# Kernel optimization log

Hardware: AMD Instinct MI355X
Metric: run time of the kernel (lower is better)

Reference implementation:

```python
import jax, jax.numpy as jnp
import numpy as np

FEATURE_DIM = 512
DEPTH = 128
NUM_CLASSES = 1000


def setup_inputs() -> dict:
    key = jax.random.key(0)
    ks = jax.random.split(key, 9)
    s = 1.0 / np.sqrt(FEATURE_DIM)
    sd = 1.0 / np.sqrt(DEPTH)
    return {
        "x": jax.random.normal(ks[0], (8, 2048, FEATURE_DIM), dtype=jnp.float32),
        "Wq": jax.random.uniform(ks[1], (FEATURE_DIM, DEPTH), jnp.float32, -s, s),
        "bq": jax.random.uniform(ks[2], (DEPTH,), jnp.float32, -s, s),
        "Wk": jax.random.uniform(ks[3], (FEATURE_DIM, DEPTH), jnp.float32, -s, s),
        "bk": jax.random.uniform(ks[4], (DEPTH,), jnp.float32, -s, s),
        "Wv": jax.random.uniform(ks[5], (FEATURE_DIM, DEPTH), jnp.float32, -s, s),
        "bv": jax.random.uniform(ks[6], (DEPTH,), jnp.float32, -s, s),
        "Wl": jax.random.uniform(ks[7], (DEPTH, NUM_CLASSES), jnp.float32, -sd, sd),
        "bl": jax.random.uniform(ks[8], (NUM_CLASSES,), jnp.float32, -sd, sd),
    }


def reference(x, Wq, bq, Wk, bk, Wv, bv, Wl, bl):
    # q,k,v: [B,S,depth]
    q = jnp.einsum("bsf,fd->bsd", x, Wq) + bq
    k = jnp.einsum("bsf,fd->bsd", x, Wk) + bk
    v = jnp.einsum("bsf,fd->bsd", x, Wv) + bv
    # NOTE: original applies no 1/sqrt(depth) scaling
    logit = jnp.einsum("bqd,bkd->bqk", q, k)  # [B,S,S]
    attn = jax.nn.softmax(logit, axis=2)
    attn_out = jnp.einsum("bqk,bkd->bqd", attn, v)  # [B,S,depth]
    out = jnp.einsum("bsd,dc->bsc", attn_out, Wl) + bl  # [B,S,C]
    return out.mean(axis=1)  # [B,C]
```

## Files before the change

### kernel.cpp

```cpp
#include <hip/hip_runtime.h>
#include <stdint.h>

#define NB 8
#define SS 2048
#define FF 512
#define DD 128
#define CC 1000
#define KC 8
#define CHUNK (SS / KC)

typedef __attribute__((ext_vector_type(8))) short bf16x8;
typedef __attribute__((ext_vector_type(4))) float f32x4;
typedef __attribute__((ext_vector_type(4))) unsigned int u32x4;

__device__ __forceinline__ short f2bf(float f) {
    uint32_t u;
    __builtin_memcpy(&u, &f, 4);
    u = (u + 0x7fffu + ((u >> 16) & 1u)) >> 16;
    return (short)u;
}
__device__ __forceinline__ float bf2f(short h) {
    uint32_t u = ((uint32_t)(uint16_t)h) << 16;
    float f;
    __builtin_memcpy(&f, &u, 4);
    return f;
}
__device__ __forceinline__ uint32_t cvtpk(float a, float b) {
    uint32_t r;
    asm("v_cvt_pk_bf16_f32 %0, %1, %2" : "=v"(r) : "v"(a), "v"(b));
    return r;
}
__device__ __forceinline__ void async16(const void* g, void* l) {
    __builtin_amdgcn_global_load_lds(
        (const __attribute__((address_space(1))) uint32_t*)g,
        (__attribute__((address_space(3))) uint32_t*)l, 16, 0, 0);
}

__global__ void prep(const float* __restrict__ Wq, const float* __restrict__ Wk,
                     const float* __restrict__ Wv, short* __restrict__ Wt)
{
    int id = blockIdx.x * 256 + threadIdx.x;
    int w = id >> 16, rem = id & 65535;
    int n = rem >> 9, kx = rem & 511;
    const float* Wsrc = (w == 0) ? Wq : (w == 1) ? Wk : Wv;
    Wt[w * 65536 + n * 512 + kx] = f2bf(Wsrc[kx * 128 + n]);
}

__global__ __launch_bounds__(256) void qkv_proj(
    const float* __restrict__ x, const short* __restrict__ Wt,
    const float* __restrict__ bq, const float* __restrict__ bk, const float* __restrict__ bv,
    short* __restrict__ qo, short* __restrict__ ko, short* __restrict__ vo)
{
    __shared__ __align__(16) short As[2][128 * 64];
    __shared__ __align__(16) short Bs[2][128 * 64];

    const int m0   = blockIdx.x * 128;
    const int mat  = blockIdx.y;
    const int tid  = threadIdx.x;
    const int wave = tid >> 6, lane = tid & 63;
    const int quad = lane >> 4, l16 = lane & 15;
    const int wr = wave >> 1, wc = wave & 1;

    const short* Wm = Wt + mat * 65536;

    f32x4 acc[4][4];
    for (int i = 0; i < 4; i++)
        for (int j = 0; j < 4; j++) acc[i][j] = (f32x4){0.f, 0.f, 0.f, 0.f};

    const int sr = lane >> 3;
    const int sc = (lane & 7) ^ (sr & 7);

    float4 a0[4], a1[4];

#define A_LOAD(kk)                                                          \
    for (int i = 0; i < 4; i++) {                                           \
        int ins = wave * 4 + i;                                             \
        int r = ins * 8 + sr;                                               \
        const float4* s4 = (const float4*)(x + (size_t)(m0 + r) * 512 + (kk) + sc * 8); \
        a0[i] = s4[0]; a1[i] = s4[1];                                       \
    }
#define A_WRITE(buf)                                                        \
    for (int i = 0; i < 4; i++) {                                           \
        int ins = wave * 4 + i;                                             \
        u32x4 p;                                                            \
        p[0] = cvtpk(a0[i].x, a0[i].y);                                     \
        p[1] = cvtpk(a0[i].z, a0[i].w);                                     \
        p[2] = cvtpk(a1[i].x, a1[i].y);                                     \
        p[3] = cvtpk(a1[i].z, a1[i].w);                                     \
        *(u32x4*)&As[buf][ins * 512 + lane * 8] = p;                        \
    }
#define B_STAGE(buf, kk)                                                    \
    for (int i = 0; i < 4; i++) {                                           \
        int ins = wave * 4 + i;                                             \
        int r = ins * 8 + sr;                                               \
        async16(Wm + r * 512 + (kk) + sc * 8, &Bs[buf][ins * 512]);         \
    }

    A_LOAD(0)
    B_STAGE(0, 0)
    A_WRITE(0)
    __syncthreads();

    int cur = 0;
    for (int t = 0; t < 8; t++) {
        if (t < 7) {
            A_LOAD((t + 1) * 64)
            B_STAGE(cur ^ 1, (t + 1) * 64)
        }

        for (int kc = 0; kc < 2; kc++) {
            bf16x8 af[4], bfr[4];
            for (int mt = 0; mt < 4; mt++) {
                int R = wr * 64 + mt * 16 + l16, cc = kc * 4 + quad;
                af[mt] = *(const bf16x8*)&As[cur][(R * 8 + (cc ^ (R & 7))) * 8];
            }
            for (int nt = 0; nt < 4; nt++) {
                int R = wc * 64 + nt * 16 + l16, cc = kc * 4 + quad;
                bfr[nt] = *(const bf16x8*)&Bs[cur][(R * 8 + (cc ^ (R & 7))) * 8];
            }
            for (int mt = 0; mt < 4; mt++)
                for (int nt = 0; nt < 4; nt++)
                    acc[mt][nt] = __builtin_amdgcn_mfma_f32_16x16x32_bf16(
                        af[mt], bfr[nt], acc[mt][nt], 0, 0, 0);
        }
        if (t < 7) { A_WRITE(cur ^ 1) }
        __syncthreads();
        cur ^= 1;
    }
#undef A_LOAD
#undef A_WRITE
#undef B_STAGE

    const float* bias = (mat == 0) ? bq : (mat == 1) ? bk : bv;
    short* outp = (mat == 0) ? qo : (mat == 1) ? ko : vo;
    for (int mt = 0; mt < 4; mt++) {
        int grow_base = m0 + wr * 64 + mt * 16 + quad * 4;
        for (int nt = 0; nt < 4; nt++) {
            int col = wc * 64 + nt * 16 + l16;
            float bb = bias[col];
            for (int r = 0; r < 4; r++)
                outp[(grow_base + r) * 128 + col] = f2bf(acc[mt][nt][r] + bb);
        }
    }
}

__global__ __launch_bounds__(256) void attn_l(
    const short* __restrict__ q, const short* __restrict__ k,
    float* __restrict__ l_part, float* __restrict__ accum)
{
    __shared__ __align__(16) short ks[2][64 * 128];

    const int b  = blockIdx.y;
    const int q0 = blockIdx.x * 128;
    const int lq = blockIdx.z;
    const int c0 = lq * CHUNK;
    const int tid  = threadIdx.x;
    const int wave = tid >> 6, lane = tid & 63;
    const int quad = lane >> 4, l16 = lane & 15;

    if (blockIdx.x == 0 && blockIdx.y == 0 && blockIdx.z == 0) {
        accum[tid] = 0.f; accum[256 + tid] = 0.f;
        accum[512 + tid] = 0.f; accum[768 + tid] = 0.f;
    }

    bf16x8 qf[2][4];
    for (int m = 0; m < 2; m++)
        for (int c = 0; c < 4; c++)
            qf[m][c] = *(const bf16x8*)(q + (b * 2048 + q0 + wave * 32 + m * 16 + l16) * 128
                                          + c * 32 + quad * 8);

    float lsum[2][4] = {{0.f,0.f,0.f,0.f},{0.f,0.f,0.f,0.f}};
    const int krl = lane >> 4;

#define K_STAGE(buf, s0)                                                     \
    for (int i = 0; i < 4; i++) {                                            \
        int ik = wave * 4 + i;                                               \
        int kr = ik * 4 + krl;                                               \
        int kc8 = (lane & 15) ^ (kr & 15);                                   \
        async16(k + (b * 2048 + (s0) + kr) * 128 + kc8 * 8, &ks[buf][ik * 512]); \
    }

    K_STAGE(0, c0)
    __syncthreads();

    int cur = 0;
    for (int t = 0; t < CHUNK / 64; t++) {
        if (t < CHUNK / 64 - 1) { K_STAGE(cur ^ 1, c0 + (t + 1) * 64) }

        for (int ct = 0; ct < 4; ct++) {
            f32x4 Sf[2];
            Sf[0] = (f32x4){0.f,0.f,0.f,0.f};
            Sf[1] = (f32x4){0.f,0.f,0.f,0.f};
            int R = ct * 16 + l16;
            __builtin_amdgcn_s_setprio(1);
            for (int c = 0; c < 4; c++) {
                int cc = c * 4 + quad;
                bf16x8 kb = *(const bf16x8*)&ks[cur][(R * 16 + (cc ^ l16)) * 8];
                for (int m = 0; m < 2; m++)
                    Sf[m] = __builtin_amdgcn_mfma_f32_16x16x32_bf16(
                        qf[m][c], kb, Sf[m], 0, 0, 0);
            }
            __builtin_amdgcn_s_setprio(0);
            for (int m = 0; m < 2; m++)
                for (int r = 0; r < 4; r++)
                    lsum[m][r] += __expf(Sf[m][r] - 10.0f);
        }
        __syncthreads();
        cur ^= 1;
    }

    for (int m = 0; m < 2; m++)
        for (int r = 0; r < 4; r++) {
            float lv = lsum[m][r];
            lv += __shfl_xor(lv, 1);
            lv += __shfl_xor(lv, 2);
            lv += __shfl_xor(lv, 4);
            lv += __shfl_xor(lv, 8);
            if (l16 == 0)
                l_part[(lq * 8 + b) * 2048 + q0 + wave * 32 + m * 16 + quad * 4 + r] = lv;
        }
}

__global__ __launch_bounds__(256) void attn_w(
    const short* __restrict__ q, const short* __restrict__ k,
    const float* __restrict__ l_part, float* __restrict__ w_part)
{
    __shared__ __align__(16) short ks[2][64 * 128];
    __shared__ float wl[4][256];

    const int b  = blockIdx.y;
    const int qt = blockIdx.x;
    const int q0 = qt * 128;
    const int lq = blockIdx.z;
    const int c0 = lq * CHUNK;
    const int tid  = threadIdx.x;
    const int wave = tid >> 6, lane = tid & 63;
    const int quad = lane >> 4, l16 = lane & 15;

    bf16x8 qf[2][4];
    for (int m = 0; m < 2; m++)
        for (int c = 0; c < 4; c++)
            qf[m][c] = *(const bf16x8*)(q + (b * 2048 + q0 + wave * 32 + m * 16 + l16) * 128
                                          + c * 32 + quad * 8);

    float linv[2][4];
    for (int m = 0; m < 2; m++)
        for (int r = 0; r < 4; r++) {
            int row = q0 + wave * 32 + m * 16 + quad * 4 + r;
            float lt = 0.f;
            for (int kc = 0; kc < KC; kc++) lt += l_part[(kc * 8 + b) * 2048 + row];
            linv[m][r] = 1.0f / lt;
        }

    const int krl = lane >> 4;

    K_STAGE(0, c0)
    __syncthreads();

    int cur = 0;
    for (int t = 0; t < CHUNK / 64; t++) {
        if (t < CHUNK / 64 - 1) { K_STAGE(cur ^ 1, c0 + (t + 1) * 64) }
        int s0 = c0 + t * 64;

        for (int ct = 0; ct < 4; ct++) {
            f32x4 Sf[2];
            Sf[0] = (f32x4){0.f,0.f,0.f,0.f};
            Sf[1] = (f32x4){0.f,0.f,0.f,0.f};
            int R = ct * 16 + l16;
            __builtin_amdgcn_s_setprio(1);
            for (int c = 0; c < 4; c++) {
                int cc = c * 4 + quad;
                bf16x8 kb = *(const bf16x8*)&ks[cur][(R * 16 + (cc ^ l16)) * 8];
                for (int m = 0; m < 2; m++)
                    Sf[m] = __builtin_amdgcn_mfma_f32_16x16x32_bf16(
                        qf[m][c], kb, Sf[m], 0, 0, 0);
            }
            __builtin_amdgcn_s_setprio(0);
            float cs = 0.f;
            for (int m = 0; m < 2; m++)
                for (int r = 0; r < 4; r++)
                    cs += __expf(Sf[m][r] - 10.0f) * linv[m][r];
            cs += __shfl_xor(cs, 16);
            cs += __shfl_xor(cs, 32);
            if (quad == 0) wl[wave][(s0 - c0) + ct * 16 + l16] = cs;
        }
        __syncthreads();
        cur ^= 1;
    }
#undef K_STAGE

    {
        float s = wl[0][tid] + wl[1][tid] + wl[2][tid] + wl[3][tid];
        w_part[(qt * 8 + b) * 2048 + c0 + tid] = s;
    }
}

__global__ __launch_bounds__(256) void wv(
    const float* __restrict__ w_part, const short* __restrict__ vo,
    float* __restrict__ accum)
{
    __shared__ float wsh[128];
    __shared__ float red[16][129];
    const int b    = blockIdx.x;
    const int slab = blockIdx.y;
    const int tid  = threadIdx.x;

    if (tid < 128) {
        int s = slab * 128 + tid;
        float wsum = 0.f;
        for (int qt = 0; qt < 16; qt++) wsum += w_part[(qt * 8 + b) * 2048 + s];
        wsh[tid] = wsum;
    }
    __syncthreads();

    const int dgrp = tid & 15, sgrp = tid >> 4;
    const int d0 = dgrp * 8;
    float a[8] = {0.f,0.f,0.f,0.f,0.f,0.f,0.f,0.f};
    for (int i = 0; i < 8; i++) {
        int sl = sgrp * 8 + i;
        bf16x8 v = *(const bf16x8*)(vo + (size_t)(b * 2048 + slab * 128 + sl) * 128 + d0);
        float w = wsh[sl];
        for (int j = 0; j < 8; j++) a[j] += w * bf2f(v[j]);
    }
    for (int j = 0; j < 8; j++) red[sgrp][d0 + j] = a[j];
    __syncthreads();

    if (tid < 128) {
        float s = 0.f;
        for (int g = 0; g < 16; g++) s += red[g][tid];
        atomicAdd(&accum[b * 128 + tid], s);
    }
}

__global__ void final_proj(const float* __restrict__ accum, const float* __restrict__ Wl,
                           const float* __restrict__ bl, float* __restrict__ out)
{
    int id = blockIdx.x * 256 + threadIdx.x;
    if (id >= NB * CC) return;
    int b = id / CC, c = id % CC;
    float s = 0.f;
    for (int d = 0; d < 128; d++)
        s += accum[b * 128 + d] * Wl[d * 1000 + c];
    out[id] = s * (1.0f / 2048.0f) + bl[c];
}

extern "C" void kernel_launch(void* const* d_in, const int* in_sizes, int n_in,
                              void* d_out, int out_size, void* d_ws, size_t ws_size,
                              hipStream_t stream) {
    const float* x  = (const float*)d_in[0];
    const float* Wq = (const float*)d_in[1];
    const float* bq = (const float*)d_in[2];
    const float* Wk = (const float*)d_in[3];
    const float* bk = (const float*)d_in[4];
    const float* Wv = (const float*)d_in[5];
    const float* bv = (const float*)d_in[6];
    const float* Wl = (const float*)d_in[7];
    const float* bl = (const float*)d_in[8];
    float* out = (float*)d_out;

    char* ws = (char*)d_ws;
    short* qo     = (short*)(ws);
    short* ko     = (short*)(ws + 4194304);
    short* vo     = (short*)(ws + 8388608);
    short* Wt     = (short*)(ws + 12582912);
    float* l_part = (float*)(ws + 12976128);
    float* w_part = (float*)(ws + 13500416);
    float* acc    = (float*)(ws + 14548992);

    prep<<<768, 256, 0, stream>>>(Wq, Wk, Wv, Wt);
    qkv_proj<<<dim3(128, 3), 256, 0, stream>>>(x, Wt, bq, bk, bv, qo, ko, vo);
    attn_l<<<dim3(16, 8, KC), 256, 0, stream>>>(qo, ko, l_part, acc);
    attn_w<<<dim3(16, 8, KC), 256, 0, stream>>>(qo, ko, l_part, w_part);
    wv<<<dim3(8, 16), 256, 0, stream>>>(w_part, vo, acc);
    final_proj<<<(NB * CC + 255) / 256, 256, 0, stream>>>(acc, Wl, bl, out);
}
```

Measured before the change: 146.1 us.

## Fuse Q/K/V projections into one kernel sharing each x tile across all three

```diff
diff --git a/kernel.cpp b/kernel.cpp
--- a/kernel.cpp
+++ b/kernel.cpp
@@ -46,54 +46,44 @@
     Wt[w * 65536 + n * 512 + kx] = f2bf(Wsrc[kx * 128 + n]);
 }
 
-__global__ __launch_bounds__(256) void qkv_proj(
+__global__ __launch_bounds__(512) void qkv_mega(
     const float* __restrict__ x, const short* __restrict__ Wt,
     const float* __restrict__ bq, const float* __restrict__ bk, const float* __restrict__ bv,
     short* __restrict__ qo, short* __restrict__ ko, short* __restrict__ vo)
 {
-    __shared__ __align__(16) short As[2][128 * 64];
-    __shared__ __align__(16) short Bs[2][128 * 64];
-
-    const int m0   = blockIdx.x * 128;
-    const int mat  = blockIdx.y;
+    __shared__ __align__(16) short As[2][64 * 64];
+    __shared__ __align__(16) short Bs[2][384 * 64];
+
+    const int m0   = blockIdx.x * 64;
     const int tid  = threadIdx.x;
     const int wave = tid >> 6, lane = tid & 63;
     const int quad = lane >> 4, l16 = lane & 15;
-    const int wr = wave >> 1, wc = wave & 1;
-
-    const short* Wm = Wt + mat * 65536;
-
-    f32x4 acc[4][4];
+
+    f32x4 acc[4][3];
     for (int i = 0; i < 4; i++)
-        for (int j = 0; j < 4; j++) acc[i][j] = (f32x4){0.f, 0.f, 0.f, 0.f};
-
-    const int sr = lane >> 3;
-    const int sc = (lane & 7) ^ (sr & 7);
-
-    float4 a0[4], a1[4];
-
-#define A_LOAD(kk)                                                          \
-    for (int i = 0; i < 4; i++) {                                           \
-        int ins = wave * 4 + i;                                             \
-        int r = ins * 8 + sr;                                               \
-        const float4* s4 = (const float4*)(x + (size_t)(m0 + r) * 512 + (kk) + sc * 8); \
-        a0[i] = s4[0]; a1[i] = s4[1];                                       \
-    }
-#define A_WRITE(buf)                                                        \
-    for (int i = 0; i < 4; i++) {                                           \
-        int ins = wave * 4 + i;                                             \
+        for (int j = 0; j < 3; j++) acc[i][j] = (f32x4){0.f, 0.f, 0.f, 0.f};
+
+    const int sr  = lane >> 3;
+    const int sc  = (lane & 7) ^ (sr & 7);
+    const int ar  = tid >> 3;
+    const int ac8 = tid & 7;
+    const int aslot = ar * 8 + (ac8 ^ (ar & 7));
+
+    float4 a0, a1;
+
+#define A_LOAD(kk) {                                                        \
+        const float4* s4 = (const float4*)(x + (size_t)(m0 + ar) * 512 + (kk) + ac8 * 8); \
+        a0 = s4[0]; a1 = s4[1]; }
+#define A_WRITE(buf) {                                                      \
         u32x4 p;                                                            \
-        p[0] = cvtpk(a0[i].x, a0[i].y);                                     \
-        p[1] = cvtpk(a0[i].z, a0[i].w);                                     \
-        p[2] = cvtpk(a1[i].x, a1[i].y);                                     \
-        p[3] = cvtpk(a1[i].z, a1[i].w);                                     \
-        *(u32x4*)&As[buf][ins * 512 + lane * 8] = p;                        \
-    }
+        p[0] = cvtpk(a0.x, a0.y); p[1] = cvtpk(a0.z, a0.w);                 \
+        p[2] = cvtpk(a1.x, a1.y); p[3] = cvtpk(a1.z, a1.w);                 \
+        *(u32x4*)&As[buf][aslot * 8] = p; }
 #define B_STAGE(buf, kk)                                                    \
-    for (int i = 0; i < 4; i++) {                                           \
-        int ins = wave * 4 + i;                                             \
-        int r = ins * 8 + sr;                                               \
-        async16(Wm + r * 512 + (kk) + sc * 8, &Bs[buf][ins * 512]);         \
+    for (int i = 0; i < 6; i++) {                                           \
+        int ins = wave * 6 + i;                                  \
+        int r = ins * 8 + sr;                                   \
+        async16(Wt + r * 512 + (kk) + sc * 8, &Bs[buf][ins * 512]);         \
     }
 
     A_LOAD(0)
@@ -109,19 +99,20 @@
         }
 
         for (int kc = 0; kc < 2; kc++) {
-            bf16x8 af[4], bfr[4];
+            bf16x8 af[4], bfr[3];
+            int cc = kc * 4 + quad;
             for (int mt = 0; mt < 4; mt++) {
-                int R = wr * 64 + mt * 16 + l16, cc = kc * 4 + quad;
+                int R = mt * 16 + l16;
                 af[mt] = *(const bf16x8*)&As[cur][(R * 8 + (cc ^ (R & 7))) * 8];
             }
-            for (int nt = 0; nt < 4; nt++) {
-                int R = wc * 64 + nt * 16 + l16, cc = kc * 4 + quad;
-                bfr[nt] = *(const bf16x8*)&Bs[cur][(R * 8 + (cc ^ (R & 7))) * 8];
+            for (int nf = 0; nf < 3; nf++) {
+                int R = wave * 48 + nf * 16 + l16;
+                bfr[nf] = *(const bf16x8*)&Bs[cur][(R * 8 + (cc ^ (R & 7))) * 8];
             }
             for (int mt = 0; mt < 4; mt++)
-                for (int nt = 0; nt < 4; nt++)
-                    acc[mt][nt] = __builtin_amdgcn_mfma_f32_16x16x32_bf16(
-                        af[mt], bfr[nt], acc[mt][nt], 0, 0, 0);
+                for (int nf = 0; nf < 3; nf++)
+                    acc[mt][nf] = __builtin_amdgcn_mfma_f32_16x16x32_bf16(
+                        af[mt], bfr[nf], acc[mt][nf], 0, 0, 0);
         }
         if (t < 7) { A_WRITE(cur ^ 1) }
         __syncthreads();
@@ -131,15 +122,18 @@
 #undef A_WRITE
 #undef B_STAGE
 
-    const float* bias = (mat == 0) ? bq : (mat == 1) ? bk : bv;
-    short* outp = (mat == 0) ? qo : (mat == 1) ? ko : vo;
-    for (int mt = 0; mt < 4; mt++) {
-        int grow_base = m0 + wr * 64 + mt * 16 + quad * 4;
-        for (int nt = 0; nt < 4; nt++) {
-            int col = wc * 64 + nt * 16 + l16;
-            float bb = bias[col];
+    const float* const bps[3] = { bq, bk, bv };
+    short* const ops[3] = { qo, ko, vo };
+    for (int nf = 0; nf < 3; nf++) {
+        int colb = wave * 48 + nf * 16;
+        int mat = colb >> 7;
+        int lc  = (colb & 127) + l16;
+        float bb = bps[mat][lc];
+        short* outp = ops[mat];
+        for (int mt = 0; mt < 4; mt++) {
+            int grow = m0 + mt * 16 + quad * 4;
             for (int r = 0; r < 4; r++)
-                outp[(grow_base + r) * 128 + col] = f2bf(acc[mt][nt][r] + bb);
+                outp[(size_t)(grow + r) * 128 + lc] = f2bf(acc[mt][nf][r] + bb);
         }
     }
 }
@@ -368,7 +362,7 @@
     float* acc    = (float*)(ws + 14548992);
 
     prep<<<768, 256, 0, stream>>>(Wq, Wk, Wv, Wt);
-    qkv_proj<<<dim3(128, 3), 256, 0, stream>>>(x, Wt, bq, bk, bv, qo, ko, vo);
+    qkv_mega<<<256, 512, 0, stream>>>(x, Wt, bq, bk, bv, qo, ko, vo);
     attn_l<<<dim3(16, 8, KC), 256, 0, stream>>>(qo, ko, l_part, acc);
     attn_w<<<dim3(16, 8, KC), 256, 0, stream>>>(qo, ko, l_part, w_part);
     wv<<<dim3(8, 16), 256, 0, stream>>>(w_part, vo, acc);
```

Result: no change. 143.9 us (-1.5%).
